# Kernel tuning notes

Hardware: AMD Instinct MI355X
Metric: run time of the kernel (lower is better)

Reference implementation:

```python
import jax, jax.numpy as jnp
import numpy as np

CHUNK = 16
GROUPS = 8
EPS = 1e-5


def setup_inputs() -> dict:
    key = jax.random.key(0)
    ks = jax.random.split(key, 8)
    B, C, H, W = 8, 1, 2048, 2048
    D_in = C * CHUNK * CHUNK  # 256
    D = 16                    # out_channels
    x = jax.random.normal(ks[0], (B, C, H, W), dtype=jnp.float32)
    s_fc = 1.0 / np.sqrt(D_in)
    fc_wr = jax.random.normal(ks[1], (D, D_in), dtype=jnp.float32) * s_fc
    fc_wi = jax.random.normal(ks[2], (D, D_in), dtype=jnp.float32) * s_fc
    fc_br = jax.random.normal(ks[3], (D,), dtype=jnp.float32) * s_fc
    fc_bi = jax.random.normal(ks[4], (D,), dtype=jnp.float32) * s_fc
    conv_w = jax.random.normal(ks[5], (D, D), dtype=jnp.float32) * (1.0 / np.sqrt(D))
    conv_b = jax.random.normal(ks[6], (D,), dtype=jnp.float32) * 0.05
    gamma = jnp.ones((D,), dtype=jnp.float32)
    beta = jnp.zeros((D,), dtype=jnp.float32)
    return {"x": x, "fc_wr": fc_wr, "fc_wi": fc_wi, "fc_br": fc_br,
            "fc_bi": fc_bi, "conv_w": conv_w, "conv_b": conv_b,
            "gamma": gamma, "beta": beta}


def reference(x, fc_wr, fc_wi, fc_br, fc_bi, conv_w, conv_b, gamma, beta):
    B, C, H, W = x.shape
    s = CHUNK
    h, w = H // s, W // s
    D = fc_wr.shape[0]
    # rearrange 'b c (h s1) (w s2) -> (b h w) (s1 s2 c)'
    p = x.reshape(B, C, h, s, w, s)
    p = p.transpose(0, 2, 4, 3, 5, 1).reshape(B * h * w, s * s * C)
    # FFT over the flattened patch dim (ortho norm) -> complex64
    fft = jnp.fft.fft(p, norm="ortho")
    Wc = fc_wr + 1j * fc_wi           # [D, D_in] complex
    bc = fc_br + 1j * fc_bi           # [D]
    fc = fft @ Wc.T + bc              # [N, D] complex linear
    # IFFT over channel dim (size D), keep real part
    y = jnp.fft.ifft(fc, norm="ortho").real  # [N, D] float32
    # '(b h w) d -> b d h w'
    y = y.reshape(B, h, w, D).transpose(0, 3, 1, 2)
    # 1x1 conv
    y = jnp.einsum("bdhw,ed->behw", y, conv_w) + conv_b[None, :, None, None]
    # GroupNorm(GROUPS, D)
    yg = y.reshape(B, GROUPS, D // GROUPS, h, w)
    mean = yg.mean(axis=(2, 3, 4), keepdims=True)
    var = yg.var(axis=(2, 3, 4), keepdims=True)
    yn = ((yg - mean) * jax.lax.rsqrt(var + EPS)).reshape(B, D, h, w)
    return yn * gamma[None, :, None, None] + beta[None, :, None, None]
```

## Files before the change

### kernel.cpp

```cpp
#include <hip/hip_runtime.h>
#include <math.h>

#define PI_F 3.14159265358979323846f


#define WS_M     0
#define WS_V     4096
#define WS_A     4352
#define WS_U     8448
#define WS_STATS 8464
#define WS_AH    8592

using half8  = __attribute__((ext_vector_type(8))) _Float16;
using floatx4 = __attribute__((ext_vector_type(4))) float;

__global__ void prep1(const float* __restrict__ wr, const float* __restrict__ wi,
                      const float* __restrict__ br, const float* __restrict__ bi,
                      float* __restrict__ M, float* __restrict__ v) {
    const int m = blockIdx.x;
    const int t = threadIdx.x;
    __shared__ float Tr[256], Ti[256], cosT[256], sinT[256], cd[16], sd[16];

    float ang = (2.0f * PI_F / 256.0f) * (float)t;
    cosT[t] = cosf(ang);
    sinT[t] = sinf(ang);
    if (t < 16) {
        float a = (2.0f * PI_F / 16.0f) * (float)((t * m) & 15);
        cd[t] = cosf(a);
        sd[t] = sinf(a);
    }
    __syncthreads();

    float tr = 0.f, ti = 0.f;
    #pragma unroll
    for (int d = 0; d < 16; ++d) {
        float wrv = wr[d * 256 + t];
        float wiv = wi[d * 256 + t];
        tr += wrv * cd[d] - wiv * sd[d];
        ti += wrv * sd[d] + wiv * cd[d];
    }
    Tr[t] = tr;
    Ti[t] = ti;
    __syncthreads();

    float acc = 0.f;
    for (int k = 0; k < 256; ++k) {
        int a = (k * t) & 255;
        acc += Tr[k] * cosT[a] + Ti[k] * sinT[a];
    }
    M[m * 256 + t] = acc * (1.0f / 64.0f);

    if (t == 0) {
        float s = 0.f;
        #pragma unroll
        for (int d = 0; d < 16; ++d) {
            float a = (2.0f * PI_F / 16.0f) * (float)((d * m) & 15);
            s += br[d] * cosf(a) - bi[d] * sinf(a);
        }
        v[m] = 0.25f * s;
    }
}

__global__ void prep2(const float* __restrict__ conv_w, const float* __restrict__ conv_b,
                      const float* __restrict__ M, const float* __restrict__ v,
                      float* __restrict__ ws) {
    const int t = threadIdx.x;
    float* A = ws + WS_A;
    _Float16* Ah = (_Float16*)(ws + WS_AH);
    __shared__ float cw[256];
    __shared__ float Ms[16][256];
    cw[t] = conv_w[t];
    #pragma unroll
    for (int m = 0; m < 16; ++m) Ms[m][t] = M[m * 256 + t];
    __syncthreads();

    #pragma unroll
    for (int e = 0; e < 16; ++e) {
        float acc = 0.f;
        #pragma unroll
        for (int m = 0; m < 16; ++m) acc += cw[e * 16 + m] * Ms[m][t];
        A[e * 256 + t] = acc;
        Ah[e * 256 + t] = (_Float16)acc;
    }
    if (t < 16) {
        float acc = conv_b[t];
        #pragma unroll
        for (int m = 0; m < 16; ++m) acc += cw[t * 16 + m] * v[m];
        ws[WS_U + t] = acc;
    }
    if (t < 128) ws[WS_STATS + t] = 0.f;
}

__global__ __launch_bounds__(256) void main_k(const float* __restrict__ x,
                                              const float* __restrict__ ws,
                                              float* __restrict__ out,
                                              float* __restrict__ stats) {
    __shared__ _Float16 A_sh[16 * 264];
    __shared__ float out_s[64 * 17];
    __shared__ float Us[16];
    __shared__ float s_sum[8], s_ssq[8];
    const int t = threadIdx.x;

    {
        const uint4* asrc = (const uint4*)(ws + WS_AH);
        uint4 q0 = asrc[t * 2];
        uint4 q1 = asrc[t * 2 + 1];
        _Float16* dp = A_sh + (t >> 4) * 264 + (t & 15) * 16;
        *(uint4*)dp       = q0;
        *(uint4*)(dp + 8) = q1;
    }
    if (t < 16) Us[t] = ws[WS_U + t];
    if (t < 8) { s_sum[t] = 0.f; s_ssq[t] = 0.f; }
    __syncthreads();

    const int w    = t >> 6;
    const int lane = t & 63;
    const int m    = lane & 15;
    const int kg   = lane >> 4;

    const int P0  = blockIdx.x << 6;
    const int b   = P0 >> 14;
    const int pi  = P0 & 16383;
    const int ph  = pi >> 7;
    const int pw0 = pi & 127;

    const float* xb = x + ((size_t)b << 22)
                        + (size_t)(ph << 4) * 2048
                        + (size_t)((pw0 + w * 16 + m) << 4);

    floatx4 acc = {0.f, 0.f, 0.f, 0.f};
    const int r_off = (kg >> 1);
    const int c_off = (kg & 1) << 3;

    #pragma unroll
    for (int s = 0; s < 8; ++s) {
        const float* px = xb + (size_t)(2 * s + r_off) * 2048 + c_off;
        float4 x0 = *(const float4*)px;
        float4 x1 = *(const float4*)(px + 4);
        half8 a;
        a[0] = (_Float16)x0.x; a[1] = (_Float16)x0.y;
        a[2] = (_Float16)x0.z; a[3] = (_Float16)x0.w;
        a[4] = (_Float16)x1.x; a[5] = (_Float16)x1.y;
        a[6] = (_Float16)x1.z; a[7] = (_Float16)x1.w;
        half8 bf = *(const half8*)&A_sh[m * 264 + s * 32 + kg * 8];
        acc = __builtin_amdgcn_mfma_f32_16x16x32_f16(a, bf, acc, 0, 0, 0);
    }

    #pragma unroll
    for (int r = 0; r < 4; ++r)
        out_s[(w * 16 + kg * 4 + r) * 17 + m] = acc[r];
    __syncthreads();

    const int ch = t >> 4;
    const int i4 = t & 15;
    const float u = Us[ch];
    float v0 = out_s[(i4 * 4 + 0) * 17 + ch] + u;
    float v1 = out_s[(i4 * 4 + 1) * 17 + ch] + u;
    float v2 = out_s[(i4 * 4 + 2) * 17 + ch] + u;
    float v3 = out_s[(i4 * 4 + 3) * 17 + ch] + u;
    *(float4*)&out[((size_t)b << 18) + (size_t)ch * 16384
                   + (size_t)(ph << 7) + (size_t)(pw0 + i4 * 4)]
        = make_float4(v0, v1, v2, v3);

    float sv = v0 + v1 + v2 + v3;
    float qv = v0 * v0 + v1 * v1 + v2 * v2 + v3 * v3;
    #pragma unroll
    for (int off = 1; off <= 16; off <<= 1) {
        sv += __shfl_xor(sv, off, 64);
        qv += __shfl_xor(qv, off, 64);
    }
    if ((lane & 31) == 0) {
        atomicAdd(&s_sum[ch >> 1], sv);
        atomicAdd(&s_ssq[ch >> 1], qv);
    }
    __syncthreads();
    if (t < 8) {
        atomicAdd(&stats[b * 8 + t],      s_sum[t]);
        atomicAdd(&stats[64 + b * 8 + t], s_ssq[t]);
    }
}

__global__ __launch_bounds__(256) void finalize(float* __restrict__ out,
                                                const float* __restrict__ stats,
                                                const float* __restrict__ gamma,
                                                const float* __restrict__ beta) {
    const int i    = blockIdx.x * 256 + threadIdx.x;
    const int flat = i << 2;
    const int b = flat >> 18;
    const int c = (flat >> 14) & 15;
    const int g = c >> 1;

    const float inv_n = 1.0f / 32768.0f;
    float mean = stats[b * 8 + g] * inv_n;
    float var  = stats[64 + b * 8 + g] * inv_n - mean * mean;
    float rstd = rsqrtf(var + 1e-5f);
    float sc = rstd * gamma[c];
    float sh = beta[c] - mean * sc;

    float4 vv = ((float4*)out)[i];
    vv.x = vv.x * sc + sh;
    vv.y = vv.y * sc + sh;
    vv.z = vv.z * sc + sh;
    vv.w = vv.w * sc + sh;
    ((float4*)out)[i] = vv;
}

extern "C" void kernel_launch(void* const* d_in, const int* in_sizes, int n_in,
                              void* d_out, int out_size, void* d_ws, size_t ws_size,
                              hipStream_t stream) {
    const float* x  = (const float*)d_in[0];
    const float* wr = (const float*)d_in[1];
    const float* wi = (const float*)d_in[2];
    const float* br = (const float*)d_in[3];
    const float* bi = (const float*)d_in[4];
    const float* cw = (const float*)d_in[5];
    const float* cb = (const float*)d_in[6];
    const float* gm = (const float*)d_in[7];
    const float* bt = (const float*)d_in[8];
    float* out = (float*)d_out;
    float* ws  = (float*)d_ws;

    prep1<<<16, 256, 0, stream>>>(wr, wi, br, bi, ws + WS_M, ws + WS_V);
    prep2<<<1, 256, 0, stream>>>(cw, cb, ws + WS_M, ws + WS_V, ws);
    main_k<<<2048, 256, 0, stream>>>(x, ws, out, ws + WS_STATS);
    finalize<<<2048, 256, 0, stream>>>(out, ws + WS_STATS, gm, bt);
}
```

Measured before the change: 227.0 us.

## Fuse weight prep kernels and write MFMA results directly without LDS transpose

```diff
diff --git a/kernel.cpp b/kernel.cpp
--- a/kernel.cpp
+++ b/kernel.cpp
@@ -4,91 +4,75 @@
 #define PI_F 3.14159265358979323846f
 
 
-#define WS_M     0
-#define WS_V     4096
-#define WS_A     4352
-#define WS_U     8448
-#define WS_STATS 8464
-#define WS_AH    8592
+#define WS_AH    0
+#define WS_U     2048
+#define WS_STATS 2112
 
-using half8  = __attribute__((ext_vector_type(8))) _Float16;
+using half8   = __attribute__((ext_vector_type(8))) _Float16;
 using floatx4 = __attribute__((ext_vector_type(4))) float;
 
-__global__ void prep1(const float* __restrict__ wr, const float* __restrict__ wi,
-                      const float* __restrict__ br, const float* __restrict__ bi,
-                      float* __restrict__ M, float* __restrict__ v) {
-    const int m = blockIdx.x;
+__global__ __launch_bounds__(256) void prep(
+        const float* __restrict__ wr, const float* __restrict__ wi,
+        const float* __restrict__ br, const float* __restrict__ bi,
+        const float* __restrict__ cw, const float* __restrict__ cb,
+        float* __restrict__ ws) {
+    const int e = blockIdx.x;
     const int t = threadIdx.x;
-    __shared__ float Tr[256], Ti[256], cosT[256], sinT[256], cd[16], sd[16];
+    __shared__ float c16[16], s16[16], Fr[16], Fi[16];
+    __shared__ float Gr[256], Gi[256], cosT[256], sinT[256];
 
     float ang = (2.0f * PI_F / 256.0f) * (float)t;
     cosT[t] = cosf(ang);
     sinT[t] = sinf(ang);
     if (t < 16) {
-        float a = (2.0f * PI_F / 16.0f) * (float)((t * m) & 15);
-        cd[t] = cosf(a);
-        sd[t] = sinf(a);
+        float a = (2.0f * PI_F / 16.0f) * (float)t;
+        c16[t] = cosf(a);
+        s16[t] = sinf(a);
     }
     __syncthreads();
 
-    float tr = 0.f, ti = 0.f;
-    #pragma unroll
-    for (int d = 0; d < 16; ++d) {
-        float wrv = wr[d * 256 + t];
-        float wiv = wi[d * 256 + t];
-        tr += wrv * cd[d] - wiv * sd[d];
-        ti += wrv * sd[d] + wiv * cd[d];
+    if (t < 16) {
+        float fr = 0.f, fi = 0.f;
+        #pragma unroll
+        for (int m = 0; m < 16; ++m) {
+            float c = cw[e * 16 + m];
+            fr += c * c16[(t * m) & 15];
+            fi += c * s16[(t * m) & 15];
+        }
+        Fr[t] = fr;
+        Fi[t] = fi;
     }
-    Tr[t] = tr;
-    Ti[t] = ti;
+    __syncthreads();
+
+    {
+        float gr = 0.f, gi = 0.f;
+        #pragma unroll
+        for (int d = 0; d < 16; ++d) {
+            float wrv = wr[d * 256 + t];
+            float wiv = wi[d * 256 + t];
+            gr += wrv * Fr[d] - wiv * Fi[d];
+            gi += wrv * Fi[d] + wiv * Fr[d];
+        }
+        Gr[t] = gr;
+        Gi[t] = gi;
+    }
+    if (t == 0) {
+        float s = 0.f;
+        #pragma unroll
+        for (int d = 0; d < 16; ++d) s += br[d] * Fr[d] - bi[d] * Fi[d];
+        ws[WS_U + e] = cb[e] + 0.25f * s;
+    }
     __syncthreads();
 
     float acc = 0.f;
     for (int k = 0; k < 256; ++k) {
         int a = (k * t) & 255;
-        acc += Tr[k] * cosT[a] + Ti[k] * sinT[a];
+        acc += Gr[k] * cosT[a] + Gi[k] * sinT[a];
     }
-    M[m * 256 + t] = acc * (1.0f / 64.0f);
+    _Float16* Ah = (_Float16*)(ws + WS_AH);
+    Ah[e * 256 + t] = (_Float16)(acc * (1.0f / 64.0f));
 
-    if (t == 0) {
-        float s = 0.f;
-        #pragma unroll
-        for (int d = 0; d < 16; ++d) {
-            float a = (2.0f * PI_F / 16.0f) * (float)((d * m) & 15);
-            s += br[d] * cosf(a) - bi[d] * sinf(a);
-        }
-        v[m] = 0.25f * s;
-    }
-}
-
-__global__ void prep2(const float* __restrict__ conv_w, const float* __restrict__ conv_b,
-                      const float* __restrict__ M, const float* __restrict__ v,
-                      float* __restrict__ ws) {
-    const int t = threadIdx.x;
-    float* A = ws + WS_A;
-    _Float16* Ah = (_Float16*)(ws + WS_AH);
-    __shared__ float cw[256];
-    __shared__ float Ms[16][256];
-    cw[t] = conv_w[t];
-    #pragma unroll
-    for (int m = 0; m < 16; ++m) Ms[m][t] = M[m * 256 + t];
-    __syncthreads();
-
-    #pragma unroll
-    for (int e = 0; e < 16; ++e) {
-        float acc = 0.f;
-        #pragma unroll
-        for (int m = 0; m < 16; ++m) acc += cw[e * 16 + m] * Ms[m][t];
-        A[e * 256 + t] = acc;
-        Ah[e * 256 + t] = (_Float16)acc;
-    }
-    if (t < 16) {
-        float acc = conv_b[t];
-        #pragma unroll
-        for (int m = 0; m < 16; ++m) acc += cw[t * 16 + m] * v[m];
-        ws[WS_U + t] = acc;
-    }
-    if (t < 128) ws[WS_STATS + t] = 0.f;
+    if (e == 0 && t < 128) ws[WS_STATS + t] = 0.f;
 }
 
 __global__ __launch_bounds__(256) void main_k(const float* __restrict__ x,
@@ -96,8 +80,6 @@
                                               float* __restrict__ out,
                                               float* __restrict__ stats) {
     __shared__ _Float16 A_sh[16 * 264];
-    __shared__ float out_s[64 * 17];
-    __shared__ float Us[16];
     __shared__ float s_sum[8], s_ssq[8];
     const int t = threadIdx.x;
 
@@ -109,14 +91,14 @@
         *(uint4*)dp       = q0;
         *(uint4*)(dp + 8) = q1;
     }
-    if (t < 16) Us[t] = ws[WS_U + t];
     if (t < 8) { s_sum[t] = 0.f; s_ssq[t] = 0.f; }
-    __syncthreads();
 
     const int w    = t >> 6;
     const int lane = t & 63;
     const int m    = lane & 15;
     const int kg   = lane >> 4;
+
+    const float u = ws[WS_U + m];
 
     const int P0  = blockIdx.x << 6;
     const int b   = P0 >> 14;
@@ -127,6 +109,7 @@
     const float* xb = x + ((size_t)b << 22)
                         + (size_t)(ph << 4) * 2048
                         + (size_t)((pw0 + w * 16 + m) << 4);
+    __syncthreads();
 
     floatx4 acc = {0.f, 0.f, 0.f, 0.f};
     const int r_off = (kg >> 1);
@@ -146,32 +129,22 @@
         acc = __builtin_amdgcn_mfma_f32_16x16x32_f16(a, bf, acc, 0, 0, 0);
     }
 
-    #pragma unroll
-    for (int r = 0; r < 4; ++r)
-        out_s[(w * 16 + kg * 4 + r) * 17 + m] = acc[r];
-    __syncthreads();
-
-    const int ch = t >> 4;
-    const int i4 = t & 15;
-    const float u = Us[ch];
-    float v0 = out_s[(i4 * 4 + 0) * 17 + ch] + u;
-    float v1 = out_s[(i4 * 4 + 1) * 17 + ch] + u;
-    float v2 = out_s[(i4 * 4 + 2) * 17 + ch] + u;
-    float v3 = out_s[(i4 * 4 + 3) * 17 + ch] + u;
-    *(float4*)&out[((size_t)b << 18) + (size_t)ch * 16384
-                   + (size_t)(ph << 7) + (size_t)(pw0 + i4 * 4)]
+    float v0 = acc[0] + u;
+    float v1 = acc[1] + u;
+    float v2 = acc[2] + u;
+    float v3 = acc[3] + u;
+    *(float4*)&out[((size_t)b << 18) + (size_t)m * 16384
+                   + (size_t)(ph << 7) + (size_t)(pw0 + w * 16 + kg * 4)]
         = make_float4(v0, v1, v2, v3);
 
     float sv = v0 + v1 + v2 + v3;
     float qv = v0 * v0 + v1 * v1 + v2 * v2 + v3 * v3;
-    #pragma unroll
-    for (int off = 1; off <= 16; off <<= 1) {
-        sv += __shfl_xor(sv, off, 64);
-        qv += __shfl_xor(qv, off, 64);
-    }
-    if ((lane & 31) == 0) {
-        atomicAdd(&s_sum[ch >> 1], sv);
-        atomicAdd(&s_ssq[ch >> 1], qv);
+    sv += __shfl_xor(sv, 16, 64);  qv += __shfl_xor(qv, 16, 64);
+    sv += __shfl_xor(sv, 32, 64);  qv += __shfl_xor(qv, 32, 64);
+    sv += __shfl_xor(sv, 1, 64);   qv += __shfl_xor(qv, 1, 64);
+    if (kg == 0 && (m & 1) == 0) {
+        atomicAdd(&s_sum[m >> 1], sv);
+        atomicAdd(&s_ssq[m >> 1], qv);
     }
     __syncthreads();
     if (t < 8) {
@@ -220,8 +193,7 @@
     float* out = (float*)d_out;
     float* ws  = (float*)d_ws;
 
-    prep1<<<16, 256, 0, stream>>>(wr, wi, br, bi, ws + WS_M, ws + WS_V);
-    prep2<<<1, 256, 0, stream>>>(cw, cb, ws + WS_M, ws + WS_V, ws);
+    prep<<<16, 256, 0, stream>>>(wr, wi, br, bi, cw, cb, ws);
     main_k<<<2048, 256, 0, stream>>>(x, ws, out, ws + WS_STATS);
     finalize<<<2048, 256, 0, stream>>>(out, ws + WS_STATS, gm, bt);
 }
```

New measurement: 223.4 us. No clear change (-1.6%).
